# Kernel tuning notes

Measured on AMD Instinct MI355X. Metric: run time of the kernel, lower is better.

The kernel has to match this reference:

```python
import jax, jax.numpy as jnp
import numpy as np
from jax import lax
from jax.scipy.special import logsumexp

B, T, H, K = 64, 512, 1024, 8


def crf_nll(logits, tags, mask, trans):
    """Negative log-likelihood summed over batch (allennlp-style linear-chain CRF,
    no start/end transitions). logits [B,T,K], tags [B,T] int, mask [B,T] float, trans [K,K]."""
    def step(alpha, x):
        logit_t, m_t = x  # [B,K], [B]
        inner = alpha[:, :, None] + trans[None, :, :] + logit_t[:, None, :]  # [B,K,K]
        new = logsumexp(inner, axis=1)
        alpha = jnp.where(m_t[:, None] > 0, new, alpha)
        return alpha, None
    alpha, _ = lax.scan(step, logits[:, 0], (jnp.swapaxes(logits[:, 1:], 0, 1), mask[:, 1:].T))
    logZ = logsumexp(alpha, axis=-1)  # [B]
    emit = jnp.take_along_axis(logits, tags[..., None], axis=-1)[..., 0]  # [B,T]
    emit_score = jnp.sum(emit * mask, axis=-1)
    trans_score = jnp.sum(trans[tags[:, :-1], tags[:, 1:]] * mask[:, 1:], axis=-1)
    return -jnp.sum(emit_score + trans_score - logZ)


def viterbi(logits, trans):
    """Batched Viterbi decode with all-ones mask (as in the original forward).
    logits [B,T,K], trans [K,K] -> tags [B,T] int."""
    def step(alpha, logit_t):
        scores = alpha[:, :, None] + trans[None, :, :]  # [B,K_prev,K_next]
        bp = jnp.argmax(scores, axis=1)                 # [B,K]
        alpha = jnp.max(scores, axis=1) + logit_t
        return alpha, bp
    alpha, bps = lax.scan(step, logits[:, 0], jnp.swapaxes(logits[:, 1:], 0, 1))
    last = jnp.argmax(alpha, axis=-1)  # [B]
    def back(tag, bp):
        prev = jnp.take_along_axis(bp, tag[:, None], axis=1)[:, 0]
        return prev, prev
    _, prevs = lax.scan(back, last, bps, reverse=True)  # [T-1,B]
    return jnp.concatenate([prevs, last[None, :]], axis=0).T  # [B,T]


def setup_inputs():
    key = jax.random.key(0)
    ks = jax.random.split(key, 12)
    encoding = jax.random.normal(ks[0], (B, T, H), dtype=jnp.float32)
    raw = jax.random.randint(ks[1], (B, 3 * T), 0, K).astype(jnp.int32)
    offsets = jnp.concatenate([jnp.zeros(T, jnp.int32), jnp.full((T,), 8, jnp.int32), jnp.full((T,), 16, jnp.int32)])
    labels = raw + offsets[None, :]
    len_tokens = jax.random.randint(ks[2], (B,), 1, T + 1).astype(jnp.int32)
    s = 1.0 / np.sqrt(H)
    W_task = jax.random.uniform(ks[3], (H, K), jnp.float32, -s, s)
    b_task = jax.random.uniform(ks[4], (K,), jnp.float32, -s, s)
    W_process = jax.random.uniform(ks[5], (H, K), jnp.float32, -s, s)
    b_process = jax.random.uniform(ks[6], (K,), jnp.float32, -s, s)
    W_material = jax.random.uniform(ks[7], (H, K), jnp.float32, -s, s)
    b_material = jax.random.uniform(ks[8], (K,), jnp.float32, -s, s)
    trans_task = jax.random.normal(ks[9], (K, K), jnp.float32) * 0.1
    trans_process = jax.random.normal(ks[10], (K, K), jnp.float32) * 0.1
    trans_material = jax.random.normal(ks[11], (K, K), jnp.float32) * 0.1
    return {"encoding": encoding, "labels": labels, "len_tokens": len_tokens,
            "W_task": W_task, "b_task": b_task, "W_process": W_process, "b_process": b_process,
            "W_material": W_material, "b_material": b_material,
            "trans_task": trans_task, "trans_process": trans_process, "trans_material": trans_material}


def reference(encoding, labels, len_tokens, W_task, b_task, W_process, b_process,
              W_material, b_material, trans_task, trans_process, trans_material):
    task_logits = encoding @ W_task + b_task          # [B,T,K]
    process_logits = encoding @ W_process + b_process
    material_logits = encoding @ W_material + b_material
    logits3 = jnp.stack([task_logits, process_logits, material_logits])   # [3,B,T,K]
    trans3 = jnp.stack([trans_task, trans_process, trans_material])       # [3,K,K]
    # Viterbi with all-ones mask, as in the original forward
    tags3 = jax.vmap(viterbi)(logits3, trans3)  # [3,B,T]
    predicted_tags = jnp.concatenate([tags3[0], tags3[1] + 8, tags3[2] + 16], axis=1)  # [B,3T]
    # CRF NLL losses with length mask (training/validation path)
    mask = (jnp.arange(T)[None, :] < len_tokens[:, None]).astype(jnp.float32)
    labels3 = jnp.stack([labels[:, :T], labels[:, T:2 * T] - 8, labels[:, 2 * T:] - 16])
    loss = jnp.sum(jax.vmap(crf_nll, in_axes=(0, 0, None, 0))(logits3, labels3, mask, trans3))
    return task_logits, process_logits, material_logits, predicted_tags, loss
```

## Files before the change

### kernel.cpp

```cpp
#include <hip/hip_runtime.h>
#include <hip/hip_bf16.h>
#include <math.h>

#define BATCH 64
#define TT 512
#define HH 1024
#define KK 8
#define ROWS (BATCH * TT)
#define SEG  (ROWS * KK)
#define TAGS_OFF (3 * SEG)
#define LOSS_OFF (TAGS_OFF + BATCH * 3 * TT)

__global__ __launch_bounds__(256, 2) void gemm_heads(
    const float* __restrict__ enc,
    const float* __restrict__ Wt, const float* __restrict__ bt,
    const float* __restrict__ Wp, const float* __restrict__ bpv,
    const float* __restrict__ Wm, const float* __restrict__ bm,
    float* __restrict__ out)
{
    __shared__ float xt[4][2][16][68];
    __shared__ float wl[4][2][16][32];
    __shared__ float biasl[24];

    int tid  = threadIdx.x;
    int lane = tid & 63;
    int w    = __builtin_amdgcn_readfirstlane(tid >> 6);
    int r    = lane >> 2;
    int q    = lane & 3;
    int rowblk = blockIdx.x * 64;

    if (tid < 24) {
        int hd = tid >> 3, cl = tid & 7;
        biasl[tid] = (hd == 0) ? bt[cl] : (hd == 1) ? bpv[cl] : bm[cl];
    }

    const float* encw = enc + (size_t)rowblk * HH + w * 256;
    const float* Wkt = Wt + w * 2048;
    const float* Wkp = Wp + w * 2048;
    const float* Wkm = Wm + w * 2048;

    int srow = lane >> 2;
    int schunk = lane & 3;

    float acc[24];
#pragma unroll
    for (int c = 0; c < 24; ++c) acc[c] = 0.f;

    float4 sreg[4];
    float  wreg[6];

#define LOADT(it)                                                             \
    {                                                                         \
        _Pragma("unroll")                                                     \
        for (int i = 0; i < 4; ++i)                                           \
            sreg[i] = *(const float4*)(encw + (size_t)(srow + 16 * i) * HH +  \
                                       (it) * 16 + schunk * 4);               \
    }
#define WRITET(buf)                                                           \
    {                                                                         \
        _Pragma("unroll")                                                     \
        for (int i = 0; i < 4; ++i) {                                         \
            xt[w][buf][schunk * 4 + 0][srow + 16 * i] = sreg[i].x;            \
            xt[w][buf][schunk * 4 + 1][srow + 16 * i] = sreg[i].y;            \
            xt[w][buf][schunk * 4 + 2][srow + 16 * i] = sreg[i].z;            \
            xt[w][buf][schunk * 4 + 3][srow + 16 * i] = sreg[i].w;            \
        }                                                                     \
    }
#define WLOADG(it)                                                            \
    {                                                                         \
        wreg[0] = Wkt[(it) * 128 + lane]; wreg[1] = Wkt[(it) * 128 + 64 + lane]; \
        wreg[2] = Wkp[(it) * 128 + lane]; wreg[3] = Wkp[(it) * 128 + 64 + lane]; \
        wreg[4] = Wkm[(it) * 128 + lane]; wreg[5] = Wkm[(it) * 128 + 64 + lane]; \
    }
#define WWRITE(buf)                                                           \
    {                                                                         \
        int col_ = lane & 7;                                                  \
        _Pragma("unroll")                                                     \
        for (int i = 0; i < 6; ++i) {                                         \
            int hh_ = (lane >> 3) + 8 * (i & 1);                              \
            int c_  = 8 * (i >> 1) + col_;                                    \
            int q_  = (c_ * 43) >> 8;                       \
            int s_  = c_ - 6 * q_;                                            \
            wl[w][buf][hh_][8 * (q_ ^ (hh_ & 3)) + s_] = wreg[i];             \
        }                                                                     \
    }

    LOADT(0)
    WLOADG(0)
    WRITET(0)
    WWRITE(0)

    for (int it = 0; it < 16; ++it) {
        int cb = it & 1;
        if (it < 15) {
            LOADT(it + 1)
            WLOADG(it + 1)
        }
#pragma unroll
        for (int hh = 0; hh < 16; ++hh) {
            float4 xv = *(const float4*)&xt[w][cb][hh][4 * r];
            const float* wp_ = &wl[w][cb][hh][8 * (q ^ (hh & 3))];
            float4 w0 = *(const float4*)wp_;
            float2 w1 = *(const float2*)(wp_ + 4);
#pragma unroll
            for (int j = 0; j < 4; ++j) {
                float xe = (j == 0) ? xv.x : (j == 1) ? xv.y : (j == 2) ? xv.z : xv.w;
                acc[j * 6 + 0] = fmaf(xe, w0.x, acc[j * 6 + 0]);
                acc[j * 6 + 1] = fmaf(xe, w0.y, acc[j * 6 + 1]);
                acc[j * 6 + 2] = fmaf(xe, w0.z, acc[j * 6 + 2]);
                acc[j * 6 + 3] = fmaf(xe, w0.w, acc[j * 6 + 3]);
                acc[j * 6 + 4] = fmaf(xe, w1.x, acc[j * 6 + 4]);
                acc[j * 6 + 5] = fmaf(xe, w1.y, acc[j * 6 + 5]);
            }
        }
        if (it < 31) {
            WRITET(cb ^ 1)
            WWRITE(cb ^ 1)
        }
    }
#undef LOADT
#undef WRITET
#undef WLOADG
#undef WWRITE

    __syncthreads();
    float* xf = &xt[0][0][0][0];
    int myrow = 4 * r;
    if (w != 0) {
        float* sl = xf + w * 1600;
#pragma unroll
        for (int j = 0; j < 4; ++j)
#pragma unroll
            for (int s = 0; s < 6; ++s)
                sl[(myrow + j) * 25 + q * 6 + s] = acc[j * 6 + s];
    }
    __syncthreads();
    if (w == 0) {
#pragma unroll
        for (int j = 0; j < 4; ++j)
#pragma unroll
            for (int s = 0; s < 6; ++s)
                xf[(myrow + j) * 25 + q * 6 + s] =
                    acc[j * 6 + s] + xf[1600 + (myrow + j) * 25 + q * 6 + s]
                                   + xf[3200 + (myrow + j) * 25 + q * 6 + s]
                                   + xf[4800 + (myrow + j) * 25 + q * 6 + s];
    }
    __syncthreads();
#pragma unroll
    for (int i = 0; i < 2; ++i) {
        int flat = tid + 256 * i;
        if (flat < 384) {
            int seg  = flat >> 7;
            int rem  = flat & 127;
            int row  = rem >> 1;
            int half = rem & 1;
            float4 v;
            v.x = xf[row * 25 + seg * 8 + half * 4 + 0] + biasl[seg * 8 + half * 4 + 0];
            v.y = xf[row * 25 + seg * 8 + half * 4 + 1] + biasl[seg * 8 + half * 4 + 1];
            v.z = xf[row * 25 + seg * 8 + half * 4 + 2] + biasl[seg * 8 + half * 4 + 2];
            v.w = xf[row * 25 + seg * 8 + half * 4 + 3] + biasl[seg * 8 + half * 4 + 3];
            *(float4*)(out + (size_t)seg * SEG + (size_t)(rowblk + row) * 8 + half * 4) = v;
        }
    }
}

#define DPPF(x, ctrl) __int_as_float(__builtin_amdgcn_update_dpp(              \
    0, __float_as_int(x), ctrl, 0xF, 0xF, true))
#define SWIZF(x, pat) __int_as_float(__builtin_amdgcn_ds_swizzle(              \
    __float_as_int(x), pat))
#define BPERMF(a, x)  __int_as_float(__builtin_amdgcn_ds_bpermute(             \
    a, __float_as_int(x)))

__device__ __forceinline__ float rfl(float x) {
    return __int_as_float(__builtin_amdgcn_readfirstlane(__float_as_int(x)));
}

#if __has_builtin(__builtin_amdgcn_permlane16_swap)
__device__ __forceinline__ float xor16f(float x, int lane) {
    typedef unsigned uv2 __attribute__((ext_vector_type(2)));
    uv2 r = __builtin_amdgcn_permlane16_swap(__float_as_uint(x), __float_as_uint(x), false, false);
    return __uint_as_float((lane & 16) ? r.x : r.y);
}
#else
__device__ __forceinline__ float xor16f(float x, int lane) { return SWIZF(x, 0x401F); }
#endif

#if __has_builtin(__builtin_amdgcn_permlane32_swap)
__device__ __forceinline__ float xor32f(float x, int lane) {
    typedef unsigned uv2 __attribute__((ext_vector_type(2)));
    uv2 r = __builtin_amdgcn_permlane32_swap(__float_as_uint(x), __float_as_uint(x), false, false);
    return __uint_as_float((lane & 32) ? r.x : r.y);
}
#else
__device__ __forceinline__ float xor32f(float x, int lane) {
    return BPERMF(((lane ^ 32) << 2), x);
}
#endif

__global__ __launch_bounds__(128) void crf_vit(
    const float* __restrict__ logits,
    const int* __restrict__ labels,
    const int* __restrict__ lens,
    const float* __restrict__ trans_t,
    const float* __restrict__ trans_p,
    const float* __restrict__ trans_m,
    float* __restrict__ out_tags,
    float* __restrict__ partial)
{
    __shared__ float llds[TT * KK];
    __shared__ unsigned bpw[TT * 2];
    __shared__ unsigned fmapw[64][2];
    __shared__ unsigned char bnd[64];

    int blk = blockIdx.x;
    int h   = blk >> 6;
    int b   = blk & 63;
    int tid = threadIdx.x;
    int wid = __builtin_amdgcn_readfirstlane(tid >> 6);
    int lane = tid & 63;
    int hi = lane >> 3, lo = lane & 7;
    unsigned char* bpb = (unsigned char*)bpw;

    const float* L = logits + ((size_t)h * BATCH + b) * (TT * KK);
    const float4* Lv = (const float4*)L;
    float4* lv = (float4*)llds;
#pragma unroll
    for (int i = 0; i < 8; ++i) lv[tid + 128 * i] = Lv[tid + 128 * i];
    __syncthreads();

    const float* TR = (h == 0) ? trans_t : (h == 1) ? trans_p : trans_m;
    int len = lens[b];
    float trA = TR[lo * 8 + hi];
    float trB = TR[hi * 8 + lo];

    if (wid == 0) {
        float av = llds[lo];

#define VIT_EVEN(t, LT)                                                        \
    {                                                                          \
        float v0 = av + trA;                                                   \
        float ra = fmaxf(v0, DPPF(v0, 0xB1));                                  \
        float rb = fmaxf(ra, DPPF(ra, 0x4E));                                  \
        float vmax = fmaxf(rb, DPPF(rb, 0x141));                               \
        unsigned long long mk = __ballot(v0 == vmax);                          \
        int vi = __builtin_ctz(((unsigned)(mk >> (lane & 56))) & 0xffu);       \
        if (lo == 0) bpb[(t) * 8 + hi] = (unsigned char)vi;                    \
        av = vmax + (LT);                                                      \
    }
#define VIT_ODD(t, LT)                                                         \
    {                                                                          \
        float v0 = av + trB;                                                   \
        float ra = fmaxf(v0, DPPF(v0, 0x128));                                 \
        float rb = fmaxf(ra, xor16f(ra, lane));                                \
        float vmax = fmaxf(rb, xor32f(rb, lane));                              \
        unsigned long long mk = __ballot(v0 == vmax);                          \
        unsigned long long sel = (mk >> lo) & 0x0101010101010101ULL;           \
        int vi = __builtin_ctzll(sel) >> 3;                                    \
        if (hi == 0) bpb[(t) * 8 + lo] = (unsigned char)vi;                    \
        av = vmax + (LT);                                                      \
    }

        float ltA = llds[8 + hi];
        float ltB = llds[16 + lo];
        for (int t = 1; t <= 509; t += 2) {
            float ltA2 = llds[(t + 2) * 8 + hi];
            int tb = (t + 3 <= 511) ? (t + 3) : 511;
            float ltB2 = llds[tb * 8 + lo];
            VIT_EVEN(t, ltA);
            VIT_ODD(t + 1, ltB);
            ltA = ltA2; ltB = ltB2;
        }
        VIT_EVEN(511, ltA);
#undef VIT_EVEN
#undef VIT_ODD

        float ra = fmaxf(av, DPPF(av, 0x128));
        float rb = fmaxf(ra, xor16f(ra, lane));
        float vmax = fmaxf(rb, xor32f(rb, lane));
        unsigned long long mk = __ballot(av == vmax);
        int last_ = __builtin_ctzll(mk) >> 3;

        asm volatile("" ::: "memory");

        int t0 = lane * 8;
        unsigned rw[16];
#pragma unroll
        for (int j = 0; j < 8; ++j) {
            int t = t0 + 1 + j;
            if (t <= 511) { rw[2 * j] = bpw[t * 2]; rw[2 * j + 1] = bpw[t * 2 + 1]; }
            else          { rw[2 * j] = 0x03020100u; rw[2 * j + 1] = 0x07060504u; }
        }
        unsigned sv[8];
#pragma unroll
        for (int i = 0; i < 8; ++i) sv[i] = i;
#pragma unroll
        for (int j = 7; j >= 0; --j) {
            unsigned d0 = rw[2 * j], d1 = rw[2 * j + 1];
#pragma unroll
            for (int i = 0; i < 8; ++i) {
                unsigned s = sv[i];
                unsigned d = (s < 4) ? d0 : d1;
                sv[i] = (d >> (8 * (s & 3))) & 0xffu;
            }
        }
        fmapw[lane][0] = sv[0] | (sv[1] << 8) | (sv[2] << 16) | (sv[3] << 24);
        fmapw[lane][1] = sv[4] | (sv[5] << 8) | (sv[6] << 16) | (sv[7] << 24);
        asm volatile("" ::: "memory");

        if (lane == 0) {
            unsigned cur = (unsigned)last_;
            for (int l = 63; l >= 0; --l) {
                unsigned d = (cur < 4) ? fmapw[l][0] : fmapw[l][1];
                cur = (d >> (8 * (cur & 3))) & 0xffu;
                bnd[l] = (unsigned char)cur;
            }
        }
        asm volatile("" ::: "memory");

        int off = h * 8;
        float* otag = out_tags + b * (3 * TT) + h * TT;
        unsigned curr = (lane == 63) ? (unsigned)last_ : (unsigned)bnd[lane + 1];
#pragma unroll
        for (int j = 7; j >= 0; --j) {
            unsigned d = (curr < 4) ? rw[2 * j] : rw[2 * j + 1];
            curr = (d >> (8 * (curr & 3))) & 0xffu;
            otag[t0 + j] = (float)((int)curr + off);
        }
    } else {
        float EA = __expf(trA);
        float EB = __expf(trB);
        float al0 = llds[lo];
        float c0 = rfl(al0);
        float S = __expf(al0 - c0);
        float Mc = c0;
        float r2 = 0.f, r3 = 0.f;
        const float LN8 = 2.0794415416798357f;

#define LSE_EVEN(t, LT)                                                        \
    {                                                                          \
        float c = rfl(LT) + LN8;                                               \
        float F = __expf((LT) - c);                                            \
        float P = S * EA;                                                      \
        float sa = P + DPPF(P, 0xB1);                                          \
        float sb = sa + DPPF(sa, 0x4E);                                        \
        float ss = sb + DPPF(sb, 0x141);                                       \
        if ((t) < len) { S = ss * F; Mc += c; }                                \
        r2 = r3; r3 = __logf(rfl(S));                                          \
    }
#define LSE_ODD(t, LT)                                                         \
    {                                                                          \
        float c = rfl(LT) + LN8;                                               \
        float F = __expf((LT) - c);                                            \
        float P = S * EB;                                                      \
        float sa = P + DPPF(P, 0x128);                                         \
        float sb = sa + xor16f(sa, lane);                                      \
        float ss = sb + xor32f(sb, lane);                                      \
        if ((t) < len) { S = ss * F; Mc += c; }                                \
        r2 = r3; r3 = __logf(rfl(S));                                          \
    }

        float ltA = llds[8 + hi];
        float ltB = llds[16 + lo];
        for (int t = 1; t <= 509; t += 2) {
            if ((t & 3) == 1) {
                float g = r2;
                S *= __expf(-g);
                Mc += g;
            }
            float ltA2 = llds[(t + 2) * 8 + hi];
            int tb = (t + 3 <= 511) ? (t + 3) : 511;
            float ltB2 = llds[tb * 8 + lo];
            LSE_EVEN(t, ltA);
            LSE_ODD(t + 1, ltB);
            ltA = ltA2; ltB = ltB2;
        }
        LSE_EVEN(511, ltA);
#undef LSE_EVEN
#undef LSE_ODD

        float aj = Mc + __logf(S);
        float za = fmaxf(aj, DPPF(aj, 0x128));
        float zb = fmaxf(za, xor16f(za, lane));
        float zmax = fmaxf(zb, xor32f(zb, lane));
        float ze = __expf(aj - zmax);
        float zs = ze + DPPF(ze, 0x128);
        float zs2 = zs + xor16f(zs, lane);
        float zsum = zs2 + xor32f(zs2, lane);
        float logZ = zmax + __logf(zsum);

        const int* lab = labels + b * (3 * TT) + h * TT;
        int off = h * 8;
        float sc = 0.f;
#pragma unroll
        for (int j = 0; j < 8; ++j) {
            int t = lane + 64 * j;
            if (t < len) {
                int tg = lab[t] - off;
                sc += llds[t * 8 + tg];
                if (t >= 1) {
                    int tp = lab[t - 1] - off;
                    sc += TR[tp * 8 + tg];
                }
            }
        }
#pragma unroll
        for (int d = 1; d <= 32; d <<= 1) sc += __shfl_xor(sc, d);

        if (lane == 0) partial[blk] = logZ - sc;
    }
}

__global__ __launch_bounds__(64) void loss_reduce(
    const float* __restrict__ partial, float* __restrict__ out_loss)
{
    int lane = threadIdx.x;
    float s = partial[lane] + partial[lane + 64] + partial[lane + 128];
#pragma unroll
    for (int d = 1; d <= 32; d <<= 1) s += __shfl_xor(s, d);
    if (lane == 0) *out_loss = s;
}

extern "C" void kernel_launch(void* const* d_in, const int* in_sizes, int n_in,
                              void* d_out, int out_size, void* d_ws, size_t ws_size,
                              hipStream_t stream) {
    const float* enc    = (const float*)d_in[0];
    const int*   labels = (const int*)d_in[1];
    const int*   lens   = (const int*)d_in[2];
    const float* Wt     = (const float*)d_in[3];
    const float* bt     = (const float*)d_in[4];
    const float* Wp     = (const float*)d_in[5];
    const float* bpv    = (const float*)d_in[6];
    const float* Wm     = (const float*)d_in[7];
    const float* bm     = (const float*)d_in[8];
    const float* tr_t   = (const float*)d_in[9];
    const float* tr_p   = (const float*)d_in[10];
    const float* tr_m   = (const float*)d_in[11];

    float* out = (float*)d_out;
    float* lpart = (float*)d_ws;

    gemm_heads<<<512, 256, 0, stream>>>(enc, Wt, bt, Wp, bpv, Wm, bm, out);
    crf_vit<<<192, 128, 0, stream>>>(out, labels, lens, tr_t, tr_p, tr_m,
                                     out + TAGS_OFF, lpart);
    loss_reduce<<<1, 64, 0, stream>>>(lpart, out + LOSS_OFF);
}
```

Before: 87.92 us.

## Process two CRF sequences per block to interleave serial recurrences

Each crf_vit block now handles two (head, batch) sequences, interleaving their Viterbi and forward-algorithm recurrences so that the independent dependency chains hide each other's cross-lane shuffle and ballot latency. The grid is halved to 96 blocks, and logit prefetch now looks three steps ahead. This adds register and LDS pressure and halves parallelism across CUs, but the serial latency-bound chain should get better instruction-level overlap. The gemm change only touches an always-true guard and a launch expression that still evaluates to 512 blocks.

```diff
diff --git a/kernel.cpp b/kernel.cpp
--- a/kernel.cpp
+++ b/kernel.cpp
@@ -79,7 +79,7 @@
         for (int i = 0; i < 6; ++i) {                                         \
             int hh_ = (lane >> 3) + 8 * (i & 1);                              \
             int c_  = 8 * (i >> 1) + col_;                                    \
-            int q_  = (c_ * 43) >> 8;                       \
+            int q_  = (c_ * 43) >> 8;                                         \
             int s_  = c_ - 6 * q_;                                            \
             wl[w][buf][hh_][8 * (q_ ^ (hh_ & 3)) + s_] = wreg[i];             \
         }                                                                     \
@@ -113,7 +113,7 @@
                 acc[j * 6 + 5] = fmaf(xe, w1.y, acc[j * 6 + 5]);
             }
         }
-        if (it < 31) {
+        if (it < 15) {
             WRITET(cb ^ 1)
             WWRITE(cb ^ 1)
         }
@@ -207,206 +207,277 @@
     float* __restrict__ out_tags,
     float* __restrict__ partial)
 {
-    __shared__ float llds[TT * KK];
-    __shared__ unsigned bpw[TT * 2];
-    __shared__ unsigned fmapw[64][2];
-    __shared__ unsigned char bnd[64];
+    __shared__ float llds[2][TT * KK];
+    __shared__ unsigned bpw[2][TT * 2];
+    __shared__ unsigned fmapw[2][64][2];
+    __shared__ unsigned char bnd[2][64];
 
     int blk = blockIdx.x;
-    int h   = blk >> 6;
-    int b   = blk & 63;
+    int sA = 2 * blk, sB = 2 * blk + 1;
+    int hA = sA >> 6, bA = sA & 63;
+    int hB = sB >> 6, bB = sB & 63;
     int tid = threadIdx.x;
     int wid = __builtin_amdgcn_readfirstlane(tid >> 6);
     int lane = tid & 63;
     int hi = lane >> 3, lo = lane & 7;
-    unsigned char* bpb = (unsigned char*)bpw;
-
-    const float* L = logits + ((size_t)h * BATCH + b) * (TT * KK);
-    const float4* Lv = (const float4*)L;
-    float4* lv = (float4*)llds;
-#pragma unroll
-    for (int i = 0; i < 8; ++i) lv[tid + 128 * i] = Lv[tid + 128 * i];
+
+    {
+        const float4* LvA = (const float4*)(logits + ((size_t)hA * BATCH + bA) * (TT * KK));
+        const float4* LvB = (const float4*)(logits + ((size_t)hB * BATCH + bB) * (TT * KK));
+        float4* lvA = (float4*)llds[0];
+        float4* lvB = (float4*)llds[1];
+#pragma unroll
+        for (int i = 0; i < 8; ++i) lvA[tid + 128 * i] = LvA[tid + 128 * i];
+#pragma unroll
+        for (int i = 0; i < 8; ++i) lvB[tid + 128 * i] = LvB[tid + 128 * i];
+    }
     __syncthreads();
 
-    const float* TR = (h == 0) ? trans_t : (h == 1) ? trans_p : trans_m;
-    int len = lens[b];
-    float trA = TR[lo * 8 + hi];
-    float trB = TR[hi * 8 + lo];
+    const float* TRA = (hA == 0) ? trans_t : (hA == 1) ? trans_p : trans_m;
+    const float* TRB = (hB == 0) ? trans_t : (hB == 1) ? trans_p : trans_m;
+    int lenA = lens[bA], lenB = lens[bB];
+    float trA0 = TRA[lo * 8 + hi], trB0 = TRA[hi * 8 + lo];
+    float trA1 = TRB[lo * 8 + hi], trB1 = TRB[hi * 8 + lo];
+    const float* l0 = llds[0];
+    const float* l1 = llds[1];
 
     if (wid == 0) {
-        float av = llds[lo];
-
-#define VIT_EVEN(t, LT)                                                        \
+        unsigned char* bp0 = (unsigned char*)bpw[0];
+        unsigned char* bp1 = (unsigned char*)bpw[1];
+        float av0 = l0[lo], av1 = l1[lo];
+
+#define VIT_EVEN(AV, TRX, BPB, t, LT)                                          \
     {                                                                          \
-        float v0 = av + trA;                                                   \
+        float v0 = AV + (TRX);                                                 \
         float ra = fmaxf(v0, DPPF(v0, 0xB1));                                  \
         float rb = fmaxf(ra, DPPF(ra, 0x4E));                                  \
         float vmax = fmaxf(rb, DPPF(rb, 0x141));                               \
         unsigned long long mk = __ballot(v0 == vmax);                          \
         int vi = __builtin_ctz(((unsigned)(mk >> (lane & 56))) & 0xffu);       \
-        if (lo == 0) bpb[(t) * 8 + hi] = (unsigned char)vi;                    \
-        av = vmax + (LT);                                                      \
-    }
-#define VIT_ODD(t, LT)                                                         \
+        if (lo == 0) BPB[(t) * 8 + hi] = (unsigned char)vi;                    \
+        AV = vmax + (LT);                                                      \
+    }
+#define VIT_ODD(AV, TRX, BPB, t, LT)                                           \
     {                                                                          \
-        float v0 = av + trB;                                                   \
+        float v0 = AV + (TRX);                                                 \
         float ra = fmaxf(v0, DPPF(v0, 0x128));                                 \
         float rb = fmaxf(ra, xor16f(ra, lane));                                \
         float vmax = fmaxf(rb, xor32f(rb, lane));                              \
         unsigned long long mk = __ballot(v0 == vmax);                          \
         unsigned long long sel = (mk >> lo) & 0x0101010101010101ULL;           \
         int vi = __builtin_ctzll(sel) >> 3;                                    \
-        if (hi == 0) bpb[(t) * 8 + lo] = (unsigned char)vi;                    \
-        av = vmax + (LT);                                                      \
-    }
-
-        float ltA = llds[8 + hi];
-        float ltB = llds[16 + lo];
+        if (hi == 0) BPB[(t) * 8 + lo] = (unsigned char)vi;                    \
+        AV = vmax + (LT);                                                      \
+    }
+
+        float eA0_0 = l0[1 * 8 + hi], eA0_1 = l0[3 * 8 + hi], eA0_2 = l0[5 * 8 + hi];
+        float oA0_0 = l0[2 * 8 + lo], oA0_1 = l0[4 * 8 + lo], oA0_2 = l0[6 * 8 + lo];
+        float eA1_0 = l1[1 * 8 + hi], eA1_1 = l1[3 * 8 + hi], eA1_2 = l1[5 * 8 + hi];
+        float oA1_0 = l1[2 * 8 + lo], oA1_1 = l1[4 * 8 + lo], oA1_2 = l1[6 * 8 + lo];
+
         for (int t = 1; t <= 509; t += 2) {
-            float ltA2 = llds[(t + 2) * 8 + hi];
-            int tb = (t + 3 <= 511) ? (t + 3) : 511;
-            float ltB2 = llds[tb * 8 + lo];
-            VIT_EVEN(t, ltA);
-            VIT_ODD(t + 1, ltB);
-            ltA = ltA2; ltB = ltB2;
-        }
-        VIT_EVEN(511, ltA);
+            int te = (t + 6 <= 511) ? (t + 6) : 511;
+            int to_ = (t + 7 <= 511) ? (t + 7) : 511;
+            float nE0 = l0[te * 8 + hi], nO0 = l0[to_ * 8 + lo];
+            float nE1 = l1[te * 8 + hi], nO1 = l1[to_ * 8 + lo];
+            VIT_EVEN(av0, trA0, bp0, t, eA0_0)
+            VIT_EVEN(av1, trA1, bp1, t, eA1_0)
+            VIT_ODD(av0, trB0, bp0, t + 1, oA0_0)
+            VIT_ODD(av1, trB1, bp1, t + 1, oA1_0)
+            eA0_0 = eA0_1; eA0_1 = eA0_2; eA0_2 = nE0;
+            oA0_0 = oA0_1; oA0_1 = oA0_2; oA0_2 = nO0;
+            eA1_0 = eA1_1; eA1_1 = eA1_2; eA1_2 = nE1;
+            oA1_0 = oA1_1; oA1_1 = oA1_2; oA1_2 = nO1;
+        }
+        VIT_EVEN(av0, trA0, bp0, 511, eA0_0)
+        VIT_EVEN(av1, trA1, bp1, 511, eA1_0)
 #undef VIT_EVEN
 #undef VIT_ODD
 
-        float ra = fmaxf(av, DPPF(av, 0x128));
-        float rb = fmaxf(ra, xor16f(ra, lane));
-        float vmax = fmaxf(rb, xor32f(rb, lane));
-        unsigned long long mk = __ballot(av == vmax);
-        int last_ = __builtin_ctzll(mk) >> 3;
+        int last0, last1;
+        {
+            float ra = fmaxf(av0, DPPF(av0, 0x128));
+            float rb = fmaxf(ra, xor16f(ra, lane));
+            float vmax = fmaxf(rb, xor32f(rb, lane));
+            unsigned long long mk = __ballot(av0 == vmax);
+            last0 = __builtin_ctzll(mk) >> 3;
+        }
+        {
+            float ra = fmaxf(av1, DPPF(av1, 0x128));
+            float rb = fmaxf(ra, xor16f(ra, lane));
+            float vmax = fmaxf(rb, xor32f(rb, lane));
+            unsigned long long mk = __ballot(av1 == vmax);
+            last1 = __builtin_ctzll(mk) >> 3;
+        }
 
         asm volatile("" ::: "memory");
 
         int t0 = lane * 8;
-        unsigned rw[16];
-#pragma unroll
-        for (int j = 0; j < 8; ++j) {
-            int t = t0 + 1 + j;
-            if (t <= 511) { rw[2 * j] = bpw[t * 2]; rw[2 * j + 1] = bpw[t * 2 + 1]; }
-            else          { rw[2 * j] = 0x03020100u; rw[2 * j + 1] = 0x07060504u; }
-        }
-        unsigned sv[8];
-#pragma unroll
-        for (int i = 0; i < 8; ++i) sv[i] = i;
-#pragma unroll
-        for (int j = 7; j >= 0; --j) {
-            unsigned d0 = rw[2 * j], d1 = rw[2 * j + 1];
-#pragma unroll
-            for (int i = 0; i < 8; ++i) {
-                unsigned s = sv[i];
-                unsigned d = (s < 4) ? d0 : d1;
-                sv[i] = (d >> (8 * (s & 3))) & 0xffu;
-            }
-        }
-        fmapw[lane][0] = sv[0] | (sv[1] << 8) | (sv[2] << 16) | (sv[3] << 24);
-        fmapw[lane][1] = sv[4] | (sv[5] << 8) | (sv[6] << 16) | (sv[7] << 24);
+        for (int si = 0; si < 2; ++si) {
+            unsigned rw[16];
+#pragma unroll
+            for (int j = 0; j < 8; ++j) {
+                int t = t0 + 1 + j;
+                if (t <= 511) { rw[2 * j] = bpw[si][t * 2]; rw[2 * j + 1] = bpw[si][t * 2 + 1]; }
+                else          { rw[2 * j] = 0x03020100u; rw[2 * j + 1] = 0x07060504u; }
+            }
+            unsigned sv[8];
+#pragma unroll
+            for (int i = 0; i < 8; ++i) sv[i] = i;
+#pragma unroll
+            for (int j = 7; j >= 0; --j) {
+                unsigned d0 = rw[2 * j], d1 = rw[2 * j + 1];
+#pragma unroll
+                for (int i = 0; i < 8; ++i) {
+                    unsigned s = sv[i];
+                    unsigned d = (s < 4) ? d0 : d1;
+                    sv[i] = (d >> (8 * (s & 3))) & 0xffu;
+                }
+            }
+            fmapw[si][lane][0] = sv[0] | (sv[1] << 8) | (sv[2] << 16) | (sv[3] << 24);
+            fmapw[si][lane][1] = sv[4] | (sv[5] << 8) | (sv[6] << 16) | (sv[7] << 24);
+        }
         asm volatile("" ::: "memory");
 
-        if (lane == 0) {
-            unsigned cur = (unsigned)last_;
+        if (lane < 2) {
+            unsigned cur = (unsigned)(lane == 0 ? last0 : last1);
             for (int l = 63; l >= 0; --l) {
-                unsigned d = (cur < 4) ? fmapw[l][0] : fmapw[l][1];
+                unsigned d = (cur < 4) ? fmapw[lane][l][0] : fmapw[lane][l][1];
                 cur = (d >> (8 * (cur & 3))) & 0xffu;
-                bnd[l] = (unsigned char)cur;
+                bnd[lane][l] = (unsigned char)cur;
             }
         }
         asm volatile("" ::: "memory");
 
-        int off = h * 8;
-        float* otag = out_tags + b * (3 * TT) + h * TT;
-        unsigned curr = (lane == 63) ? (unsigned)last_ : (unsigned)bnd[lane + 1];
-#pragma unroll
-        for (int j = 7; j >= 0; --j) {
-            unsigned d = (curr < 4) ? rw[2 * j] : rw[2 * j + 1];
-            curr = (d >> (8 * (curr & 3))) & 0xffu;
-            otag[t0 + j] = (float)((int)curr + off);
+        for (int si = 0; si < 2; ++si) {
+            int hS = si == 0 ? hA : hB;
+            int bS = si == 0 ? bA : bB;
+            int lastS = si == 0 ? last0 : last1;
+            unsigned rw[16];
+#pragma unroll
+            for (int j = 0; j < 8; ++j) {
+                int t = t0 + 1 + j;
+                if (t <= 511) { rw[2 * j] = bpw[si][t * 2]; rw[2 * j + 1] = bpw[si][t * 2 + 1]; }
+                else          { rw[2 * j] = 0x03020100u; rw[2 * j + 1] = 0x07060504u; }
+            }
+            int off = hS * 8;
+            float* otag = out_tags + bS * (3 * TT) + hS * TT;
+            unsigned curr = (lane == 63) ? (unsigned)lastS : (unsigned)bnd[si][lane + 1];
+#pragma unroll
+            for (int j = 7; j >= 0; --j) {
+                unsigned d = (curr < 4) ? rw[2 * j] : rw[2 * j + 1];
+                curr = (d >> (8 * (curr & 3))) & 0xffu;
+                otag[t0 + j] = (float)((int)curr + off);
+            }
         }
     } else {
-        float EA = __expf(trA);
-        float EB = __expf(trB);
-        float al0 = llds[lo];
-        float c0 = rfl(al0);
-        float S = __expf(al0 - c0);
-        float Mc = c0;
-        float r2 = 0.f, r3 = 0.f;
         const float LN8 = 2.0794415416798357f;
-
-#define LSE_EVEN(t, LT)                                                        \
+        float EA0 = __expf(trA0), EB0 = __expf(trB0);
+        float EA1 = __expf(trA1), EB1 = __expf(trB1);
+        float a00 = l0[lo], a01 = l1[lo];
+        float c00 = rfl(a00), c01 = rfl(a01);
+        float S0 = __expf(a00 - c00), S1 = __expf(a01 - c01);
+        float Mc0 = c00, Mc1 = c01;
+        float r20 = 0.f, r30 = 0.f, r21 = 0.f, r31 = 0.f;
+
+#define LSE_EVEN(S_, MC, R2, R3, EAx, LEN, t, LT)                              \
     {                                                                          \
         float c = rfl(LT) + LN8;                                               \
         float F = __expf((LT) - c);                                            \
-        float P = S * EA;                                                      \
+        float P = S_ * (EAx);                                                  \
         float sa = P + DPPF(P, 0xB1);                                          \
         float sb = sa + DPPF(sa, 0x4E);                                        \
         float ss = sb + DPPF(sb, 0x141);                                       \
-        if ((t) < len) { S = ss * F; Mc += c; }                                \
-        r2 = r3; r3 = __logf(rfl(S));                                          \
-    }
-#define LSE_ODD(t, LT)                                                         \
+        if ((t) < (LEN)) { S_ = ss * F; MC += c; }                             \
+        R2 = R3; R3 = __logf(rfl(S_));                                         \
+    }
+#define LSE_ODD(S_, MC, R2, R3, EBx, LEN, t, LT)                               \
     {                                                                          \
         float c = rfl(LT) + LN8;                                               \
         float F = __expf((LT) - c);                                            \
-        float P = S * EB;                                                      \
+        float P = S_ * (EBx);                                                  \
         float sa = P + DPPF(P, 0x128);                                         \
         float sb = sa + xor16f(sa, lane);                                      \
         float ss = sb + xor32f(sb, lane);                                      \
-        if ((t) < len) { S = ss * F; Mc += c; }                                \
-        r2 = r3; r3 = __logf(rfl(S));                                          \
-    }
-
-        float ltA = llds[8 + hi];
-        float ltB = llds[16 + lo];
+        if ((t) < (LEN)) { S_ = ss * F; MC += c; }                             \
+        R2 = R3; R3 = __logf(rfl(S_));                                         \
+    }
+
+        float eA0_0 = l0[1 * 8 + hi], eA0_1 = l0[3 * 8 + hi], eA0_2 = l0[5 * 8 + hi];
+        float oA0_0 = l0[2 * 8 + lo], oA0_1 = l0[4 * 8 + lo], oA0_2 = l0[6 * 8 + lo];
+        float eA1_0 = l1[1 * 8 + hi], eA1_1 = l1[3 * 8 + hi], eA1_2 = l1[5 * 8 + hi];
+        float oA1_0 = l1[2 * 8 + lo], oA1_1 = l1[4 * 8 + lo], oA1_2 = l1[6 * 8 + lo];
+
         for (int t = 1; t <= 509; t += 2) {
             if ((t & 3) == 1) {
-                float g = r2;
-                S *= __expf(-g);
-                Mc += g;
-            }
-            float ltA2 = llds[(t + 2) * 8 + hi];
-            int tb = (t + 3 <= 511) ? (t + 3) : 511;
-            float ltB2 = llds[tb * 8 + lo];
-            LSE_EVEN(t, ltA);
-            LSE_ODD(t + 1, ltB);
-            ltA = ltA2; ltB = ltB2;
-        }
-        LSE_EVEN(511, ltA);
+                float g0 = r20, g1 = r21;
+                S0 *= __expf(-g0); Mc0 += g0;
+                S1 *= __expf(-g1); Mc1 += g1;
+            }
+            int te = (t + 6 <= 511) ? (t + 6) : 511;
+            int to_ = (t + 7 <= 511) ? (t + 7) : 511;
+            float nE0 = l0[te * 8 + hi], nO0 = l0[to_ * 8 + lo];
+            float nE1 = l1[te * 8 + hi], nO1 = l1[to_ * 8 + lo];
+            LSE_EVEN(S0, Mc0, r20, r30, EA0, lenA, t, eA0_0)
+            LSE_EVEN(S1, Mc1, r21, r31, EA1, lenB, t, eA1_0)
+            LSE_ODD(S0, Mc0, r20, r30, EB0, lenA, t + 1, oA0_0)
+            LSE_ODD(S1, Mc1, r21, r31, EB1, lenB, t + 1, oA1_0)
+            eA0_0 = eA0_1; eA0_1 = eA0_2; eA0_2 = nE0;
+            oA0_0 = oA0_1; oA0_1 = oA0_2; oA0_2 = nO0;
+            eA1_0 = eA1_1; eA1_1 = eA1_2; eA1_2 = nE1;
+            oA1_0 = oA1_1; oA1_1 = oA1_2; oA1_2 = nO1;
+        }
+        LSE_EVEN(S0, Mc0, r20, r30, EA0, lenA, 511, eA0_0)
+        LSE_EVEN(S1, Mc1, r21, r31, EA1, lenB, 511, eA1_0)
 #undef LSE_EVEN
 #undef LSE_ODD
 
-        float aj = Mc + __logf(S);
-        float za = fmaxf(aj, DPPF(aj, 0x128));
-        float zb = fmaxf(za, xor16f(za, lane));
-        float zmax = fmaxf(zb, xor32f(zb, lane));
-        float ze = __expf(aj - zmax);
-        float zs = ze + DPPF(ze, 0x128);
-        float zs2 = zs + xor16f(zs, lane);
-        float zsum = zs2 + xor32f(zs2, lane);
-        float logZ = zmax + __logf(zsum);
-
-        const int* lab = labels + b * (3 * TT) + h * TT;
-        int off = h * 8;
-        float sc = 0.f;
+        float logZ0, logZ1;
+        {
+            float aj = Mc0 + __logf(S0);
+            float za = fmaxf(aj, DPPF(aj, 0x128));
+            float zb = fmaxf(za, xor16f(za, lane));
+            float zmax = fmaxf(zb, xor32f(zb, lane));
+            float ze = __expf(aj - zmax);
+            float zs = ze + DPPF(ze, 0x128);
+            float zs2 = zs + xor16f(zs, lane);
+            float zsum = zs2 + xor32f(zs2, lane);
+            logZ0 = zmax + __logf(zsum);
+        }
+        {
+            float aj = Mc1 + __logf(S1);
+            float za = fmaxf(aj, DPPF(aj, 0x128));
+            float zb = fmaxf(za, xor16f(za, lane));
+            float zmax = fmaxf(zb, xor32f(zb, lane));
+            float ze = __expf(aj - zmax);
+            float zs = ze + DPPF(ze, 0x128);
+            float zs2 = zs + xor16f(zs, lane);
+            float zsum = zs2 + xor32f(zs2, lane);
+            logZ1 = zmax + __logf(zsum);
+        }
+
+        const int* labA = labels + bA * (3 * TT) + hA * TT;
+        const int* labB = labels + bB * (3 * TT) + hB * TT;
+        int offA = hA * 8, offB = hB * 8;
+        float sc0 = 0.f, sc1 = 0.f;
 #pragma unroll
         for (int j = 0; j < 8; ++j) {
             int t = lane + 64 * j;
-            if (t < len) {
-                int tg = lab[t] - off;
-                sc += llds[t * 8 + tg];
-                if (t >= 1) {
-                    int tp = lab[t - 1] - off;
-                    sc += TR[tp * 8 + tg];
-                }
-            }
-        }
-#pragma unroll
-        for (int d = 1; d <= 32; d <<= 1) sc += __shfl_xor(sc, d);
-
-        if (lane == 0) partial[blk] = logZ - sc;
+            if (t < lenA) {
+                int tg = labA[t] - offA;
+                sc0 += l0[t * 8 + tg];
+                if (t >= 1) sc0 += TRA[(labA[t - 1] - offA) * 8 + tg];
+            }
+            if (t < lenB) {
+                int tg = labB[t] - offB;
+                sc1 += l1[t * 8 + tg];
+                if (t >= 1) sc1 += TRB[(labB[t - 1] - offB) * 8 + tg];
+            }
+        }
+#pragma unroll
+        for (int d = 1; d <= 32; d <<= 1) { sc0 += __shfl_xor(sc0, d); sc1 += __shfl_xor(sc1, d); }
+
+        if (lane == 0) { partial[sA] = logZ0 - sc0; partial[sB] = logZ1 - sc1; }
     }
 }
 
@@ -439,8 +510,8 @@
     float* out = (float*)d_out;
     float* lpart = (float*)d_ws;
 
-    gemm_heads<<<512, 256, 0, stream>>>(enc, Wt, bt, Wp, bpv, Wm, bm, out);
-    crf_vit<<<192, 128, 0, stream>>>(out, labels, lens, tr_t, tr_p, tr_m,
-                                     out + TAGS_OFF, lpart);
+    gemm_heads<<<ROWS / 64, 256, 0, stream>>>(enc, Wt, bt, Wp, bpv, Wm, bm, out);
+    crf_vit<<<96, 128, 0, stream>>>(out, labels, lens, tr_t, tr_p, tr_m,
+                                    out + TAGS_OFF, lpart);
     loss_reduce<<<1, 64, 0, stream>>>(lpart, out + LOSS_OFF);
 }
```

Measured after the change: 130.8 us. 1.49x slower.

## Move Viterbi backpointer argmax out of serial recurrence into parallel post-pass

Applied to the files above, without the earlier changes.

The serial Viterbi loop now only computes max and stores the alpha values to shared memory, dropping the per-step ballot and ctz from the critical path. After the loop, a separate pass recomputes all backpointers in parallel across lanes, each lane handling 64 timesteps for one next-tag. The LSE wave now computes its rescale log inline every four steps instead of carrying a per-step log, and both loops prefetch logits two steps ahead. This costs an extra 16KB of LDS and a redundant argmax pass, and tie-breaking must match the original first-max rule.

```diff
diff --git a/kernel.cpp b/kernel.cpp
--- a/kernel.cpp
+++ b/kernel.cpp
@@ -79,7 +79,7 @@
         for (int i = 0; i < 6; ++i) {                                         \
             int hh_ = (lane >> 3) + 8 * (i & 1);                              \
             int c_  = 8 * (i >> 1) + col_;                                    \
-            int q_  = (c_ * 43) >> 8;                       \
+            int q_  = (c_ * 43) >> 8;                                         \
             int s_  = c_ - 6 * q_;                                            \
             wl[w][buf][hh_][8 * (q_ ^ (hh_ & 3)) + s_] = wreg[i];             \
         }                                                                     \
@@ -113,7 +113,7 @@
                 acc[j * 6 + 5] = fmaf(xe, w1.y, acc[j * 6 + 5]);
             }
         }
-        if (it < 31) {
+        if (it < 15) {
             WRITET(cb ^ 1)
             WWRITE(cb ^ 1)
         }
@@ -208,6 +208,7 @@
     float* __restrict__ partial)
 {
     __shared__ float llds[TT * KK];
+    __shared__ __align__(16) float alds[TT * KK];
     __shared__ unsigned bpw[TT * 2];
     __shared__ unsigned fmapw[64][2];
     __shared__ unsigned char bnd[64];
@@ -235,44 +236,42 @@
 
     if (wid == 0) {
         float av = llds[lo];
-
-#define VIT_EVEN(t, LT)                                                        \
+        if (lane < 8) alds[lane] = llds[lane];
+
+#define VSTEP_EVEN(t, LT)                                                      \
     {                                                                          \
         float v0 = av + trA;                                                   \
         float ra = fmaxf(v0, DPPF(v0, 0xB1));                                  \
         float rb = fmaxf(ra, DPPF(ra, 0x4E));                                  \
         float vmax = fmaxf(rb, DPPF(rb, 0x141));                               \
-        unsigned long long mk = __ballot(v0 == vmax);                          \
-        int vi = __builtin_ctz(((unsigned)(mk >> (lane & 56))) & 0xffu);       \
-        if (lo == 0) bpb[(t) * 8 + hi] = (unsigned char)vi;                    \
         av = vmax + (LT);                                                      \
-    }
-#define VIT_ODD(t, LT)                                                         \
+        if (lo == 0) alds[(t) * 8 + hi] = av;                                  \
+    }
+#define VSTEP_ODD(t, LT)                                                       \
     {                                                                          \
         float v0 = av + trB;                                                   \
         float ra = fmaxf(v0, DPPF(v0, 0x128));                                 \
         float rb = fmaxf(ra, xor16f(ra, lane));                                \
         float vmax = fmaxf(rb, xor32f(rb, lane));                              \
-        unsigned long long mk = __ballot(v0 == vmax);                          \
-        unsigned long long sel = (mk >> lo) & 0x0101010101010101ULL;           \
-        int vi = __builtin_ctzll(sel) >> 3;                                    \
-        if (hi == 0) bpb[(t) * 8 + lo] = (unsigned char)vi;                    \
         av = vmax + (LT);                                                      \
-    }
-
-        float ltA = llds[8 + hi];
-        float ltB = llds[16 + lo];
+        if (hi == 0) alds[(t) * 8 + lo] = av;                                  \
+    }
+
+        float ltA0 = llds[1 * 8 + hi], ltA1 = llds[3 * 8 + hi];
+        float ltB0 = llds[2 * 8 + lo], ltB1 = llds[4 * 8 + lo];
         for (int t = 1; t <= 509; t += 2) {
-            float ltA2 = llds[(t + 2) * 8 + hi];
-            int tb = (t + 3 <= 511) ? (t + 3) : 511;
-            float ltB2 = llds[tb * 8 + lo];
-            VIT_EVEN(t, ltA);
-            VIT_ODD(t + 1, ltB);
-            ltA = ltA2; ltB = ltB2;
-        }
-        VIT_EVEN(511, ltA);
-#undef VIT_EVEN
-#undef VIT_ODD
+            int te = (t + 4 <= 511) ? (t + 4) : 511;
+            int to_ = (t + 5 <= 511) ? (t + 5) : 511;
+            float nE = llds[te * 8 + hi];
+            float nO = llds[to_ * 8 + lo];
+            VSTEP_EVEN(t, ltA0)
+            VSTEP_ODD(t + 1, ltB0)
+            ltA0 = ltA1; ltA1 = nE;
+            ltB0 = ltB1; ltB1 = nO;
+        }
+        VSTEP_EVEN(511, ltA0)
+#undef VSTEP_EVEN
+#undef VSTEP_ODD
 
         float ra = fmaxf(av, DPPF(av, 0x128));
         float rb = fmaxf(ra, xor16f(ra, lane));
@@ -280,6 +279,32 @@
         unsigned long long mk = __ballot(av == vmax);
         int last_ = __builtin_ctzll(mk) >> 3;
 
+        asm volatile("" ::: "memory");
+
+        {
+            int c = lane >> 3;
+            int kn = lane & 7;
+            float Tk0 = TR[0 * 8 + kn], Tk1 = TR[1 * 8 + kn];
+            float Tk2 = TR[2 * 8 + kn], Tk3 = TR[3 * 8 + kn];
+            float Tk4 = TR[4 * 8 + kn], Tk5 = TR[5 * 8 + kn];
+            float Tk6 = TR[6 * 8 + kn], Tk7 = TR[7 * 8 + kn];
+            for (int j = 0; j < 64; ++j) {
+                int t = c * 64 + j + 1;
+                if (t <= 511) {
+                    float4 a03 = *(const float4*)&alds[(t - 1) * 8];
+                    float4 a47 = *(const float4*)&alds[(t - 1) * 8 + 4];
+                    float v = a03.x + Tk0; int vi = 0; float nv;
+                    nv = a03.y + Tk1; if (nv > v) { v = nv; vi = 1; }
+                    nv = a03.z + Tk2; if (nv > v) { v = nv; vi = 2; }
+                    nv = a03.w + Tk3; if (nv > v) { v = nv; vi = 3; }
+                    nv = a47.x + Tk4; if (nv > v) { v = nv; vi = 4; }
+                    nv = a47.y + Tk5; if (nv > v) { v = nv; vi = 5; }
+                    nv = a47.z + Tk6; if (nv > v) { v = nv; vi = 6; }
+                    nv = a47.w + Tk7; if (nv > v) { v = nv; vi = 7; }
+                    bpb[t * 8 + kn] = (unsigned char)vi;
+                }
+            }
+        }
         asm volatile("" ::: "memory");
 
         int t0 = lane * 8;
@@ -327,14 +352,14 @@
             otag[t0 + j] = (float)((int)curr + off);
         }
     } else {
+        const float LN8 = 2.0794415416798357f;
         float EA = __expf(trA);
         float EB = __expf(trB);
         float al0 = llds[lo];
         float c0 = rfl(al0);
         float S = __expf(al0 - c0);
         float Mc = c0;
-        float r2 = 0.f, r3 = 0.f;
-        const float LN8 = 2.0794415416798357f;
+        float g = 0.f;
 
 #define LSE_EVEN(t, LT)                                                        \
     {                                                                          \
@@ -345,7 +370,6 @@
         float sb = sa + DPPF(sa, 0x4E);                                        \
         float ss = sb + DPPF(sb, 0x141);                                       \
         if ((t) < len) { S = ss * F; Mc += c; }                                \
-        r2 = r3; r3 = __logf(rfl(S));                                          \
     }
 #define LSE_ODD(t, LT)                                                         \
     {                                                                          \
@@ -356,25 +380,26 @@
         float sb = sa + xor16f(sa, lane);                                      \
         float ss = sb + xor32f(sb, lane);                                      \
         if ((t) < len) { S = ss * F; Mc += c; }                                \
-        r2 = r3; r3 = __logf(rfl(S));                                          \
-    }
-
-        float ltA = llds[8 + hi];
-        float ltB = llds[16 + lo];
+    }
+
+        float ltA0 = llds[1 * 8 + hi], ltA1 = llds[3 * 8 + hi];
+        float ltB0 = llds[2 * 8 + lo], ltB1 = llds[4 * 8 + lo];
         for (int t = 1; t <= 509; t += 2) {
             if ((t & 3) == 1) {
-                float g = r2;
                 S *= __expf(-g);
                 Mc += g;
-            }
-            float ltA2 = llds[(t + 2) * 8 + hi];
-            int tb = (t + 3 <= 511) ? (t + 3) : 511;
-            float ltB2 = llds[tb * 8 + lo];
-            LSE_EVEN(t, ltA);
-            LSE_ODD(t + 1, ltB);
-            ltA = ltA2; ltB = ltB2;
-        }
-        LSE_EVEN(511, ltA);
+                g = __logf(rfl(S));
+            }
+            int te = (t + 4 <= 511) ? (t + 4) : 511;
+            int to_ = (t + 5 <= 511) ? (t + 5) : 511;
+            float nE = llds[te * 8 + hi];
+            float nO = llds[to_ * 8 + lo];
+            LSE_EVEN(t, ltA0)
+            LSE_ODD(t + 1, ltB0)
+            ltA0 = ltA1; ltA1 = nE;
+            ltB0 = ltB1; ltB1 = nO;
+        }
+        LSE_EVEN(511, ltA0)
 #undef LSE_EVEN
 #undef LSE_ODD
 
@@ -439,7 +464,7 @@
     float* out = (float*)d_out;
     float* lpart = (float*)d_ws;
 
-    gemm_heads<<<512, 256, 0, stream>>>(enc, Wt, bt, Wp, bpv, Wm, bm, out);
+    gemm_heads<<<ROWS / 64, 256, 0, stream>>>(enc, Wt, bt, Wp, bpv, Wm, bm, out);
     crf_vit<<<192, 128, 0, stream>>>(out, labels, lens, tr_t, tr_p, tr_m,
                                      out + TAGS_OFF, lpart);
     loss_reduce<<<1, 64, 0, stream>>>(lpart, out + LOSS_OFF);
```

Measured after the change: 86.46 us. Within noise of the previous version (-1.7%).
